# Performance work log

Hardware: AMD Instinct MI355X
Metric: run time of the kernel (lower is better)

Reference implementation:

```python
import jax, jax.numpy as jnp
import numpy as np

N = 50000
E = 1600000
R = 4
D_IN = 128
D_OUT = 128


def setup_inputs() -> dict:
    key = jax.random.key(0)
    ks = jax.random.split(key, 7)
    x = jax.random.normal(ks[0], (N, D_IN), dtype=jnp.float32)
    vals = jax.random.normal(ks[1], (R, E), dtype=jnp.float32) * (1.0 / 32.0)
    weight = jax.random.normal(ks[2], (D_IN, D_OUT), dtype=jnp.float32) * (1.0 / np.sqrt(D_IN))
    filt = jax.random.uniform(ks[3], (R * N, 1), dtype=jnp.float32, minval=0.9, maxval=1.1)
    bias = jnp.zeros((D_OUT,), dtype=jnp.float32)
    rows = jax.random.randint(ks[4], (R, E), 0, N, dtype=jnp.int32)
    cols = jax.random.randint(ks[5], (R, E), 0, N, dtype=jnp.int32)
    return {"x": x, "vals": vals, "weight": weight, "filt": filt,
            "bias": bias, "rows": rows, "cols": cols}


def _spmm(rows, cols, vals, h, n):
    # sparse [n,n] @ dense [n,d] via gather + segment_sum
    return jax.ops.segment_sum(vals[:, None] * h[cols], rows, num_segments=n)


def reference(x, vals, weight, filt, bias, rows, cols):
    n = x.shape[0]
    h = x @ weight                                    # [N, out]
    # cat(d_list, dim=0) @ h  ->  stack of D_i @ h, i.e. [R, N, out]
    y = jax.vmap(lambda r, c, v: _spmm(r, c, v, h, n))(rows, cols, vals)
    y = filt.reshape(rows.shape[0], n, 1) * y         # elementwise wavelet filter
    # cat(d_list, dim=1) @ y  ->  sum_i D_i @ y_i
    out = jax.vmap(lambda r, c, v, yy: _spmm(r, c, v, yy, n))(rows, cols, vals, y).sum(axis=0)
    return out + bias
```

## Files before the change

kernel.cpp:

```cpp
#include <hip/hip_runtime.h>

#define N_NODES 50000
#define N_EDGES 1600000
#define R_WAV 4
#define D 128
#define NB 391
#define CHUNK 4096
#define NPBLK ((N_EDGES + CHUNK - 1) / CHUNK)
#define MAXB 4800

typedef unsigned int u32;
typedef unsigned short u16;

static __device__ inline u16 f2bf(float f) {
    u32 u = __float_as_uint(f);
    u = (u + 0x7FFFu + ((u >> 16) & 1u)) >> 16;
    return (u16)u;
}
static __device__ inline float bf_lo(u32 u) { return __uint_as_float(u << 16); }
static __device__ inline float bf_hi(u32 u) { return __uint_as_float(u & 0xFFFF0000u); }

__global__ __launch_bounds__(128) void gemm_xw(const float* __restrict__ x,
                                               const float* __restrict__ W,
                                               u16* __restrict__ h) {
    __shared__ float xs[4 * 128];
    const int j = threadIdx.x;
    const int row0 = blockIdx.x * 4;
    for (int t = j; t < 512; t += 128) xs[t] = x[(size_t)row0 * D + t];
    __syncthreads();
    float a0 = 0.f, a1 = 0.f, a2 = 0.f, a3 = 0.f;
#pragma unroll 8
    for (int k = 0; k < 128; ++k) {
        const float w = W[k * D + j];
        a0 += xs[k] * w;
        a1 += xs[128 + k] * w;
        a2 += xs[256 + k] * w;
        a3 += xs[384 + k] * w;
    }
    h[(size_t)(row0 + 0) * D + j] = f2bf(a0);
    h[(size_t)(row0 + 1) * D + j] = f2bf(a1);
    h[(size_t)(row0 + 2) * D + j] = f2bf(a2);
    h[(size_t)(row0 + 3) * D + j] = f2bf(a3);
}

__global__ __launch_bounds__(256) void bucket_hist_all(const int* __restrict__ rows_all,
                                                       int* __restrict__ cnt4) {
    __shared__ int lh[NB];
    const int r = blockIdx.y;
    const int* rows = rows_all + (size_t)r * N_EDGES;
    int* cnt = cnt4 + r * NB;
    const int tid = threadIdx.x;
    for (int i = tid; i < NB; i += 256) lh[i] = 0;
    __syncthreads();
    const int e0 = blockIdx.x * CHUNK;
    const int e1 = min(e0 + CHUNK, N_EDGES);
    for (int i = e0 + tid; i < e1; i += 256) atomicAdd(&lh[rows[i] >> 7], 1);
    __syncthreads();
    for (int i = tid; i < NB; i += 256) {
        const int c = lh[i];
        if (c) atomicAdd(&cnt[i], c);
    }
}

__global__ __launch_bounds__(512) void scan_buckets_all(const int* __restrict__ cnt4,
                                                        int* __restrict__ bptr4,
                                                        int* __restrict__ bcur4) {
    __shared__ int sa[512], sb[512];
    const int r = blockIdx.x;
    const int* cnt = cnt4 + r * NB;
    int* bptr = bptr4 + r * (NB + 1);
    int* bcur = bcur4 + r * NB;
    const int tid = threadIdx.x;
    const int v = (tid < NB) ? cnt[tid] : 0;
    sa[tid] = v;
    int* cur = sa;
    int* nxt = sb;
    for (int d = 1; d < 512; d <<= 1) {
        __syncthreads();
        int t = cur[tid];
        if (tid >= d) t += cur[tid - d];
        nxt[tid] = t;
        int* tmp = cur; cur = nxt; nxt = tmp;
    }
    __syncthreads();
    const int excl = cur[tid] - v;
    if (tid <= NB) bptr[tid] = excl;
    if (tid < NB) bcur[tid] = excl;
}

__global__ __launch_bounds__(256) void partition_kernel(const int* __restrict__ rows,
                                                        const int* __restrict__ cols,
                                                        const float* __restrict__ vals,
                                                        int* __restrict__ bcur,
                                                        int2* __restrict__ cv) {
    __shared__ int lh[NB], lptr[NB], lcur[NB], lbase[NB];
    __shared__ int sa[256], sb[256];
    __shared__ int2 st[CHUNK];
    const int tid = threadIdx.x;
    for (int i = tid; i < NB; i += 256) lh[i] = 0;
    __syncthreads();
    const int e0 = blockIdx.x * CHUNK;
    const int e1 = min(e0 + CHUNK, N_EDGES);
    const int cnt = e1 - e0;
    for (int i = e0 + tid; i < e1; i += 256) atomicAdd(&lh[rows[i] >> 7], 1);
    __syncthreads();
    const int p0 = (2 * tid < NB) ? lh[2 * tid] : 0;
    const int p1 = (2 * tid + 1 < NB) ? lh[2 * tid + 1] : 0;
    sa[tid] = p0 + p1;
    int* cur = sa;
    int* nxt = sb;
    for (int d = 1; d < 256; d <<= 1) {
        __syncthreads();
        int t = cur[tid];
        if (tid >= d) t += cur[tid - d];
        nxt[tid] = t;
        int* tmp = cur; cur = nxt; nxt = tmp;
    }
    __syncthreads();
    const int pe = cur[tid] - (p0 + p1);
    if (2 * tid < NB)     { lptr[2 * tid] = pe;           lcur[2 * tid] = pe; }
    if (2 * tid + 1 < NB) { lptr[2 * tid + 1] = pe + p0;  lcur[2 * tid + 1] = pe + p0; }
    __syncthreads();
    for (int i = e0 + tid; i < e1; i += 256) {
        const int row = rows[i];
        const int b = row >> 7;
        const int pos = atomicAdd(&lcur[b], 1);
        st[pos] = make_int2((int)(((u32)row << 16) | (u32)cols[i]), __float_as_int(vals[i]));
    }
    __syncthreads();
    for (int b = tid; b < NB; b += 256) {
        const int c = lh[b];
        int gb = 0;
        if (c) gb = atomicAdd(&bcur[b], c);
        lbase[b] = gb - lptr[b];
    }
    __syncthreads();
    for (int i = tid; i < cnt; i += 256) {
        const int2 e = st[i];
        const int b = (int)((u32)e.x >> 23);
        cv[lbase[b] + i] = e;
    }
}

__global__ __launch_bounds__(256) void bucket_csr(const int* __restrict__ bptr,
                                                  const int2* __restrict__ cv,
                                                  u32* __restrict__ cv4,
                                                  int* __restrict__ row_ptr) {
    __shared__ int lh[128], lexcl[128], lcur[128];
    __shared__ u32 st[MAXB];
    const int b = blockIdx.x;
    const int s = bptr[b], e1 = bptr[b + 1];
    const int cnt = e1 - s;
    const int tid = threadIdx.x;
    if (tid < 128) lh[tid] = 0;
    __syncthreads();
    for (int i = s + tid; i < e1; i += 256)
        atomicAdd(&lh[((u32)cv[i].x >> 16) & 127u], 1);
    __syncthreads();
    if (tid < 64) {
        const int p0 = lh[2 * tid], p1 = lh[2 * tid + 1];
        int ssum = p0 + p1;
#pragma unroll
        for (int d = 1; d < 64; d <<= 1) {
            const int t = __shfl_up(ssum, d, 64);
            if (tid >= d) ssum += t;
        }
        const int pe = ssum - (p0 + p1);
        lexcl[2 * tid] = pe;          lcur[2 * tid] = pe;
        lexcl[2 * tid + 1] = pe + p0; lcur[2 * tid + 1] = pe + p0;
    }
    __syncthreads();
    for (int i = s + tid; i < e1; i += 256) {
        const int2 E = cv[i];
        const int lr = (int)(((u32)E.x >> 16) & 127u);
        const int pos = atomicAdd(&lcur[lr], 1);
        if (pos < MAXB)
            st[pos] = ((u32)f2bf(__int_as_float(E.y)) << 16) | ((u32)E.x & 0xFFFFu);
    }
    __syncthreads();
    const int wb = (cnt < MAXB) ? cnt : MAXB;
    for (int i = tid; i < wb; i += 256) cv4[s + i] = st[i];
    if (tid < 128) {
        const int row = (b << 7) + tid;
        if (row < N_NODES) row_ptr[row] = s + lexcl[tid];
    }
    if (b == 0 && tid == 0) row_ptr[N_NODES] = N_EDGES;
}

__global__ __launch_bounds__(256) void spmm1(const int* __restrict__ row_ptr,
                                             const u32* __restrict__ cvp,
                                             const u32* __restrict__ h2,
                                             const float* __restrict__ filt_r,
                                             u32* __restrict__ y2) {
    const int row = __builtin_amdgcn_readfirstlane(blockIdx.x * 4 + (threadIdx.x >> 6));
    const int lane = threadIdx.x & 63;
    const int half = lane >> 5;
    const int l = lane & 31;
    int e = row_ptr[row];
    const int end = row_ptr[row + 1];
    float a0 = 0.f, a1 = 0.f, a2 = 0.f, a3 = 0.f;
    float b0 = 0.f, b1 = 0.f, b2 = 0.f, b3 = 0.f;
    for (; e + 8 <= end; e += 8) {
        const u32 c0 = cvp[e], c1 = cvp[e + 1], c2 = cvp[e + 2], c3 = cvp[e + 3];
        const u32 c4 = cvp[e + 4], c5 = cvp[e + 5], c6 = cvp[e + 6], c7 = cvp[e + 7];
        const u32 uA = half ? c1 : c0;
        const u32 uB = half ? c3 : c2;
        const u32 uC = half ? c5 : c4;
        const u32 uD = half ? c7 : c6;
        const uint2 gA = *(const uint2*)(h2 + (uA & 0xFFFFu) * 64 + 2 * l);
        const uint2 gB = *(const uint2*)(h2 + (uB & 0xFFFFu) * 64 + 2 * l);
        const uint2 gC = *(const uint2*)(h2 + (uC & 0xFFFFu) * 64 + 2 * l);
        const uint2 gD = *(const uint2*)(h2 + (uD & 0xFFFFu) * 64 + 2 * l);
        const float vA = __uint_as_float(uA & 0xFFFF0000u);
        const float vB = __uint_as_float(uB & 0xFFFF0000u);
        const float vC = __uint_as_float(uC & 0xFFFF0000u);
        const float vD = __uint_as_float(uD & 0xFFFF0000u);
        a0 += vA * bf_lo(gA.x); a1 += vA * bf_hi(gA.x);
        a2 += vA * bf_lo(gA.y); a3 += vA * bf_hi(gA.y);
        b0 += vB * bf_lo(gB.x); b1 += vB * bf_hi(gB.x);
        b2 += vB * bf_lo(gB.y); b3 += vB * bf_hi(gB.y);
        a0 += vC * bf_lo(gC.x); a1 += vC * bf_hi(gC.x);
        a2 += vC * bf_lo(gC.y); a3 += vC * bf_hi(gC.y);
        b0 += vD * bf_lo(gD.x); b1 += vD * bf_hi(gD.x);
        b2 += vD * bf_lo(gD.y); b3 += vD * bf_hi(gD.y);
    }
    for (; e < end; e += 2) {
        const u32 c0 = cvp[e];
        const u32 c1 = (e + 1 < end) ? cvp[e + 1] : 0u;
        const u32 uA = half ? c1 : c0;
        const uint2 gA = *(const uint2*)(h2 + (uA & 0xFFFFu) * 64 + 2 * l);
        const float vA = __uint_as_float(uA & 0xFFFF0000u);
        a0 += vA * bf_lo(gA.x); a1 += vA * bf_hi(gA.x);
        a2 += vA * bf_lo(gA.y); a3 += vA * bf_hi(gA.y);
    }
    a0 += b0; a1 += b1; a2 += b2; a3 += b3;
    a0 += __shfl_xor(a0, 32, 64);
    a1 += __shfl_xor(a1, 32, 64);
    a2 += __shfl_xor(a2, 32, 64);
    a3 += __shfl_xor(a3, 32, 64);
    const float f = filt_r[row];
    if (half == 0) {
        uint2 o;
        o.x = (u32)f2bf(f * a0) | ((u32)f2bf(f * a1) << 16);
        o.y = (u32)f2bf(f * a2) | ((u32)f2bf(f * a3) << 16);
        *(uint2*)(y2 + (size_t)row * 64 + 2 * l) = o;
    }
}

template <bool FIRST>
__global__ __launch_bounds__(256) void spmm2(const int* __restrict__ row_ptr,
                                             const u32* __restrict__ cvp,
                                             const u32* __restrict__ y2,
                                             const float* __restrict__ bias,
                                             float* __restrict__ out) {
    const int row = __builtin_amdgcn_readfirstlane(blockIdx.x * 4 + (threadIdx.x >> 6));
    const int lane = threadIdx.x & 63;
    const int half = lane >> 5;
    const int l = lane & 31;
    int e = row_ptr[row];
    const int end = row_ptr[row + 1];
    float a0 = 0.f, a1 = 0.f, a2 = 0.f, a3 = 0.f;
    float b0 = 0.f, b1 = 0.f, b2 = 0.f, b3 = 0.f;
    for (; e + 8 <= end; e += 8) {
        const u32 c0 = cvp[e], c1 = cvp[e + 1], c2 = cvp[e + 2], c3 = cvp[e + 3];
        const u32 c4 = cvp[e + 4], c5 = cvp[e + 5], c6 = cvp[e + 6], c7 = cvp[e + 7];
        const u32 uA = half ? c1 : c0;
        const u32 uB = half ? c3 : c2;
        const u32 uC = half ? c5 : c4;
        const u32 uD = half ? c7 : c6;
        const uint2 gA = *(const uint2*)(y2 + (uA & 0xFFFFu) * 64 + 2 * l);
        const uint2 gB = *(const uint2*)(y2 + (uB & 0xFFFFu) * 64 + 2 * l);
        const uint2 gC = *(const uint2*)(y2 + (uC & 0xFFFFu) * 64 + 2 * l);
        const uint2 gD = *(const uint2*)(y2 + (uD & 0xFFFFu) * 64 + 2 * l);
        const float vA = __uint_as_float(uA & 0xFFFF0000u);
        const float vB = __uint_as_float(uB & 0xFFFF0000u);
        const float vC = __uint_as_float(uC & 0xFFFF0000u);
        const float vD = __uint_as_float(uD & 0xFFFF0000u);
        a0 += vA * bf_lo(gA.x); a1 += vA * bf_hi(gA.x);
        a2 += vA * bf_lo(gA.y); a3 += vA * bf_hi(gA.y);
        b0 += vB * bf_lo(gB.x); b1 += vB * bf_hi(gB.x);
        b2 += vB * bf_lo(gB.y); b3 += vB * bf_hi(gB.y);
        a0 += vC * bf_lo(gC.x); a1 += vC * bf_hi(gC.x);
        a2 += vC * bf_lo(gC.y); a3 += vC * bf_hi(gC.y);
        b0 += vD * bf_lo(gD.x); b1 += vD * bf_hi(gD.x);
        b2 += vD * bf_lo(gD.y); b3 += vD * bf_hi(gD.y);
    }
    for (; e < end; e += 2) {
        const u32 c0 = cvp[e];
        const u32 c1 = (e + 1 < end) ? cvp[e + 1] : 0u;
        const u32 uA = half ? c1 : c0;
        const uint2 gA = *(const uint2*)(y2 + (uA & 0xFFFFu) * 64 + 2 * l);
        const float vA = __uint_as_float(uA & 0xFFFF0000u);
        a0 += vA * bf_lo(gA.x); a1 += vA * bf_hi(gA.x);
        a2 += vA * bf_lo(gA.y); a3 += vA * bf_hi(gA.y);
    }
    a0 += b0; a1 += b1; a2 += b2; a3 += b3;
    a0 += __shfl_xor(a0, 32, 64);
    a1 += __shfl_xor(a1, 32, 64);
    a2 += __shfl_xor(a2, 32, 64);
    a3 += __shfl_xor(a3, 32, 64);
    if (half == 0) {
        float* op = out + (size_t)row * D + 4 * l;
        if (FIRST) {
            const float4 bb = *(const float4*)(bias + 4 * l);
            *(float4*)op = make_float4(a0 + bb.x, a1 + bb.y, a2 + bb.z, a3 + bb.w);
        } else {
            const float4 cc = *(const float4*)op;
            *(float4*)op = make_float4(cc.x + a0, cc.y + a1, cc.z + a2, cc.w + a3);
        }
    }
}

extern "C" void kernel_launch(void* const* d_in, const int* in_sizes, int n_in,
                              void* d_out, int out_size, void* d_ws, size_t ws_size,
                              hipStream_t stream) {
    const float* x    = (const float*)d_in[0];
    const float* vals = (const float*)d_in[1];
    const float* W    = (const float*)d_in[2];
    const float* filt = (const float*)d_in[3];
    const float* bias = (const float*)d_in[4];
    const int*   rows = (const int*)d_in[5];
    const int*   cols = (const int*)d_in[6];
    float* out = (float*)d_out;

    char* ws = (char*)d_ws;
    u16*  h       = (u16*)(ws);
    u32*  y2      = (u32*)(ws + 12800000);
    int2* cv8     = (int2*)(ws + 25600000);
    u32*  cv4     = (u32*)(ws + 38400000);
    int*  row_ptr = (int*)(ws + 44800512);
    int*  cnt4    = (int*)(ws + 45000576);
    int*  bptr4   = (int*)(ws + 45006976);
    int*  bcur4   = (int*)(ws + 45013376);

    gemm_xw<<<N_NODES / 4, 128, 0, stream>>>(x, W, h);

    hipMemsetAsync(cnt4, 0, 4 * NB * sizeof(int), stream);
    bucket_hist_all<<<dim3(NPBLK, R_WAV), 256, 0, stream>>>(rows, cnt4);
    scan_buckets_all<<<R_WAV, 512, 0, stream>>>(cnt4, bptr4, bcur4);

    for (int r = 0; r < R_WAV; ++r) {
        const int*   rows_r = rows + (size_t)r * N_EDGES;
        const int*   cols_r = cols + (size_t)r * N_EDGES;
        const float* vals_r = vals + (size_t)r * N_EDGES;
        const float* filt_r = filt + (size_t)r * N_NODES;

        partition_kernel<<<NPBLK, 256, 0, stream>>>(rows_r, cols_r, vals_r,
                                                    bcur4 + r * NB, cv8);
        bucket_csr<<<NB, 256, 0, stream>>>(bptr4 + r * (NB + 1), cv8, cv4, row_ptr);
        spmm1<<<N_NODES / 4, 256, 0, stream>>>(row_ptr, cv4, (const u32*)h, filt_r, y2);
        if (r == 0)
            spmm2<true><<<N_NODES / 4, 256, 0, stream>>>(row_ptr, cv4, y2, bias, out);
        else
            spmm2<false><<<N_NODES / 4, 256, 0, stream>>>(row_ptr, cv4, y2, bias, out);
    }
}
```

Baseline: 734.2 us.

## Batch all wavelets per launch and fuse second SpMM across wavelets

When the workspace is large enough, partition, CSR build and the first SpMM run for all four wavelets in single launches via blockIdx.y, with per-wavelet buffers. The second SpMM is fused into one kernel that loops over the four wavelets per row, accumulates in registers and writes the output once, instead of four read-modify-write passes over the output. The GEMM is also changed to compute 16 rows per block reading x directly rather than 4 rows via shared memory. The cost is a much larger workspace, and a fallback keeps the old per-wavelet path when it is too small.

```diff
diff --git a/kernel.cpp b/kernel.cpp
--- a/kernel.cpp
+++ b/kernel.cpp
@@ -8,6 +8,7 @@
 #define CHUNK 4096
 #define NPBLK ((N_EDGES + CHUNK - 1) / CHUNK)
 #define MAXB 4800
+#define RP_STRIDE 50016
 
 typedef unsigned int u32;
 typedef unsigned short u16;
@@ -23,24 +24,20 @@
 __global__ __launch_bounds__(128) void gemm_xw(const float* __restrict__ x,
                                                const float* __restrict__ W,
                                                u16* __restrict__ h) {
-    __shared__ float xs[4 * 128];
     const int j = threadIdx.x;
-    const int row0 = blockIdx.x * 4;
-    for (int t = j; t < 512; t += 128) xs[t] = x[(size_t)row0 * D + t];
-    __syncthreads();
-    float a0 = 0.f, a1 = 0.f, a2 = 0.f, a3 = 0.f;
-#pragma unroll 8
+    const int row0 = blockIdx.x * 16;
+    const float* xr = x + (size_t)row0 * D;
+    float acc[16];
+#pragma unroll
+    for (int r = 0; r < 16; ++r) acc[r] = 0.f;
+#pragma unroll 4
     for (int k = 0; k < 128; ++k) {
         const float w = W[k * D + j];
-        a0 += xs[k] * w;
-        a1 += xs[128 + k] * w;
-        a2 += xs[256 + k] * w;
-        a3 += xs[384 + k] * w;
-    }
-    h[(size_t)(row0 + 0) * D + j] = f2bf(a0);
-    h[(size_t)(row0 + 1) * D + j] = f2bf(a1);
-    h[(size_t)(row0 + 2) * D + j] = f2bf(a2);
-    h[(size_t)(row0 + 3) * D + j] = f2bf(a3);
+#pragma unroll
+        for (int r = 0; r < 16; ++r) acc[r] += xr[r * D + k] * w;
+    }
+#pragma unroll
+    for (int r = 0; r < 16; ++r) h[(size_t)(row0 + r) * D + j] = f2bf(acc[r]);
 }
 
 __global__ __launch_bounds__(256) void bucket_hist_all(const int* __restrict__ rows_all,
@@ -93,6 +90,12 @@
                                                         const float* __restrict__ vals,
                                                         int* __restrict__ bcur,
                                                         int2* __restrict__ cv) {
+    const int r = blockIdx.y;
+    rows += (size_t)r * N_EDGES;
+    cols += (size_t)r * N_EDGES;
+    vals += (size_t)r * N_EDGES;
+    bcur += r * NB;
+    cv   += (size_t)r * N_EDGES;
     __shared__ int lh[NB], lptr[NB], lcur[NB], lbase[NB];
     __shared__ int sa[256], sb[256];
     __shared__ int2 st[CHUNK];
@@ -146,6 +149,11 @@
                                                   const int2* __restrict__ cv,
                                                   u32* __restrict__ cv4,
                                                   int* __restrict__ row_ptr) {
+    const int r = blockIdx.y;
+    bptr    += r * (NB + 1);
+    cv      += (size_t)r * N_EDGES;
+    cv4     += (size_t)r * N_EDGES;
+    row_ptr += r * RP_STRIDE;
     __shared__ int lh[128], lexcl[128], lcur[128];
     __shared__ u32 st[MAXB];
     const int b = blockIdx.x;
@@ -184,14 +192,19 @@
         const int row = (b << 7) + tid;
         if (row < N_NODES) row_ptr[row] = s + lexcl[tid];
     }
-    if (b == 0 && tid == 0) row_ptr[N_NODES] = N_EDGES;
+    if (blockIdx.x == 0 && tid == 0) row_ptr[N_NODES] = N_EDGES;
 }
 
 __global__ __launch_bounds__(256) void spmm1(const int* __restrict__ row_ptr,
                                              const u32* __restrict__ cvp,
                                              const u32* __restrict__ h2,
-                                             const float* __restrict__ filt_r,
+                                             const float* __restrict__ filt,
                                              u32* __restrict__ y2) {
+    const int r = blockIdx.y;
+    row_ptr += r * RP_STRIDE;
+    cvp     += (size_t)r * N_EDGES;
+    filt    += (size_t)r * N_NODES;
+    y2      += (size_t)r * (N_NODES * 64);
     const int row = __builtin_amdgcn_readfirstlane(blockIdx.x * 4 + (threadIdx.x >> 6));
     const int lane = threadIdx.x & 63;
     const int half = lane >> 5;
@@ -238,12 +251,75 @@
     a1 += __shfl_xor(a1, 32, 64);
     a2 += __shfl_xor(a2, 32, 64);
     a3 += __shfl_xor(a3, 32, 64);
-    const float f = filt_r[row];
+    const float f = filt[row];
     if (half == 0) {
         uint2 o;
         o.x = (u32)f2bf(f * a0) | ((u32)f2bf(f * a1) << 16);
         o.y = (u32)f2bf(f * a2) | ((u32)f2bf(f * a3) << 16);
         *(uint2*)(y2 + (size_t)row * 64 + 2 * l) = o;
+    }
+}
+
+__global__ __launch_bounds__(256) void spmm2_fused(const int* __restrict__ rp_all,
+                                                   const u32* __restrict__ cv4_all,
+                                                   const u32* __restrict__ y2_all,
+                                                   const float* __restrict__ bias,
+                                                   float* __restrict__ out) {
+    const int row = __builtin_amdgcn_readfirstlane(blockIdx.x * 4 + (threadIdx.x >> 6));
+    const int lane = threadIdx.x & 63;
+    const int half = lane >> 5;
+    const int l = lane & 31;
+    float a0 = 0.f, a1 = 0.f, a2 = 0.f, a3 = 0.f;
+    float b0 = 0.f, b1 = 0.f, b2 = 0.f, b3 = 0.f;
+    for (int r = 0; r < R_WAV; ++r) {
+        const int* rp = rp_all + r * RP_STRIDE;
+        const u32* cvp = cv4_all + (size_t)r * N_EDGES;
+        const u32* y2 = y2_all + (size_t)r * (N_NODES * 64);
+        int e = rp[row];
+        const int end = rp[row + 1];
+        for (; e + 8 <= end; e += 8) {
+            const u32 c0 = cvp[e], c1 = cvp[e + 1], c2 = cvp[e + 2], c3 = cvp[e + 3];
+            const u32 c4 = cvp[e + 4], c5 = cvp[e + 5], c6 = cvp[e + 6], c7 = cvp[e + 7];
+            const u32 uA = half ? c1 : c0;
+            const u32 uB = half ? c3 : c2;
+            const u32 uC = half ? c5 : c4;
+            const u32 uD = half ? c7 : c6;
+            const uint2 gA = *(const uint2*)(y2 + (uA & 0xFFFFu) * 64 + 2 * l);
+            const uint2 gB = *(const uint2*)(y2 + (uB & 0xFFFFu) * 64 + 2 * l);
+            const uint2 gC = *(const uint2*)(y2 + (uC & 0xFFFFu) * 64 + 2 * l);
+            const uint2 gD = *(const uint2*)(y2 + (uD & 0xFFFFu) * 64 + 2 * l);
+            const float vA = __uint_as_float(uA & 0xFFFF0000u);
+            const float vB = __uint_as_float(uB & 0xFFFF0000u);
+            const float vC = __uint_as_float(uC & 0xFFFF0000u);
+            const float vD = __uint_as_float(uD & 0xFFFF0000u);
+            a0 += vA * bf_lo(gA.x); a1 += vA * bf_hi(gA.x);
+            a2 += vA * bf_lo(gA.y); a3 += vA * bf_hi(gA.y);
+            b0 += vB * bf_lo(gB.x); b1 += vB * bf_hi(gB.x);
+            b2 += vB * bf_lo(gB.y); b3 += vB * bf_hi(gB.y);
+            a0 += vC * bf_lo(gC.x); a1 += vC * bf_hi(gC.x);
+            a2 += vC * bf_lo(gC.y); a3 += vC * bf_hi(gC.y);
+            b0 += vD * bf_lo(gD.x); b1 += vD * bf_hi(gD.x);
+            b2 += vD * bf_lo(gD.y); b3 += vD * bf_hi(gD.y);
+        }
+        for (; e < end; e += 2) {
+            const u32 c0 = cvp[e];
+            const u32 c1 = (e + 1 < end) ? cvp[e + 1] : 0u;
+            const u32 uA = half ? c1 : c0;
+            const uint2 gA = *(const uint2*)(y2 + (uA & 0xFFFFu) * 64 + 2 * l);
+            const float vA = __uint_as_float(uA & 0xFFFF0000u);
+            a0 += vA * bf_lo(gA.x); a1 += vA * bf_hi(gA.x);
+            a2 += vA * bf_lo(gA.y); a3 += vA * bf_hi(gA.y);
+        }
+    }
+    a0 += b0; a1 += b1; a2 += b2; a3 += b3;
+    a0 += __shfl_xor(a0, 32, 64);
+    a1 += __shfl_xor(a1, 32, 64);
+    a2 += __shfl_xor(a2, 32, 64);
+    a3 += __shfl_xor(a3, 32, 64);
+    if (half == 0) {
+        const float4 bb = *(const float4*)(bias + 4 * l);
+        *(float4*)(out + (size_t)row * D + 4 * l) =
+            make_float4(a0 + bb.x, a1 + bb.y, a2 + bb.z, a3 + bb.w);
     }
 }
 
@@ -324,34 +400,63 @@
     float* out = (float*)d_out;
 
     char* ws = (char*)d_ws;
-    u16*  h       = (u16*)(ws);
-    u32*  y2      = (u32*)(ws + 12800000);
-    int2* cv8     = (int2*)(ws + 25600000);
-    u32*  cv4     = (u32*)(ws + 38400000);
-    int*  row_ptr = (int*)(ws + 44800512);
-    int*  cnt4    = (int*)(ws + 45000576);
-    int*  bptr4   = (int*)(ws + 45006976);
-    int*  bcur4   = (int*)(ws + 45013376);
-
-    gemm_xw<<<N_NODES / 4, 128, 0, stream>>>(x, W, h);
-
-    hipMemsetAsync(cnt4, 0, 4 * NB * sizeof(int), stream);
-    bucket_hist_all<<<dim3(NPBLK, R_WAV), 256, 0, stream>>>(rows, cnt4);
-    scan_buckets_all<<<R_WAV, 512, 0, stream>>>(cnt4, bptr4, bcur4);
-
-    for (int r = 0; r < R_WAV; ++r) {
-        const int*   rows_r = rows + (size_t)r * N_EDGES;
-        const int*   cols_r = cols + (size_t)r * N_EDGES;
-        const float* vals_r = vals + (size_t)r * N_EDGES;
-        const float* filt_r = filt + (size_t)r * N_NODES;
-
-        partition_kernel<<<NPBLK, 256, 0, stream>>>(rows_r, cols_r, vals_r,
-                                                    bcur4 + r * NB, cv8);
-        bucket_csr<<<NB, 256, 0, stream>>>(bptr4 + r * (NB + 1), cv8, cv4, row_ptr);
-        spmm1<<<N_NODES / 4, 256, 0, stream>>>(row_ptr, cv4, (const u32*)h, filt_r, y2);
-        if (r == 0)
-            spmm2<true><<<N_NODES / 4, 256, 0, stream>>>(row_ptr, cv4, y2, bias, out);
-        else
-            spmm2<false><<<N_NODES / 4, 256, 0, stream>>>(row_ptr, cv4, y2, bias, out);
-    }
-}
+    const size_t NEED_BATCHED = 90419968;
+
+    if (ws_size >= NEED_BATCHED) {
+        u16*  h   = (u16*)(ws);
+        u32*  sh  = (u32*)(ws + 12800000);
+        int2* cv8 = (int2*)sh;
+        u32*  y2  = sh;
+        u32*  cv4 = (u32*)(ws + 64000000);
+        int*  rp  = (int*)(ws + 89600000);
+        int*  cnt4  = (int*)(ws + 90400512);
+        int*  bptr4 = (int*)(ws + 90406912);
+        int*  bcur4 = (int*)(ws + 90413312);
+
+        gemm_xw<<<N_NODES / 16, 128, 0, stream>>>(x, W, h);
+
+        hipMemsetAsync(cnt4, 0, 4 * NB * sizeof(int), stream);
+        bucket_hist_all<<<dim3(NPBLK, R_WAV), 256, 0, stream>>>(rows, cnt4);
+        scan_buckets_all<<<R_WAV, 512, 0, stream>>>(cnt4, bptr4, bcur4);
+
+        partition_kernel<<<dim3(NPBLK, R_WAV), 256, 0, stream>>>(rows, cols, vals,
+                                                                 bcur4, cv8);
+        bucket_csr<<<dim3(NB, R_WAV), 256, 0, stream>>>(bptr4, cv8, cv4, rp);
+        spmm1<<<dim3(N_NODES / 4, R_WAV), 256, 0, stream>>>(rp, cv4, (const u32*)h,
+                                                            filt, y2);
+        spmm2_fused<<<N_NODES / 4, 256, 0, stream>>>(rp, cv4, y2, bias, out);
+    } else {
+        u16*  h       = (u16*)(ws);
+        u32*  y2      = (u32*)(ws + 12800000);
+        int2* cv8     = (int2*)(ws + 25600000);
+        u32*  cv4     = (u32*)(ws + 38400000);
+        int*  row_ptr = (int*)(ws + 44800512);
+        int*  cnt4    = (int*)(ws + 45000576);
+        int*  bptr4   = (int*)(ws + 45006976);
+        int*  bcur4   = (int*)(ws + 45013376);
+
+        gemm_xw<<<N_NODES / 16, 128, 0, stream>>>(x, W, h);
+
+        hipMemsetAsync(cnt4, 0, 4 * NB * sizeof(int), stream);
+        bucket_hist_all<<<dim3(NPBLK, R_WAV), 256, 0, stream>>>(rows, cnt4);
+        scan_buckets_all<<<R_WAV, 512, 0, stream>>>(cnt4, bptr4, bcur4);
+
+        for (int r = 0; r < R_WAV; ++r) {
+            const int*   rows_r = rows + (size_t)r * N_EDGES;
+            const int*   cols_r = cols + (size_t)r * N_EDGES;
+            const float* vals_r = vals + (size_t)r * N_EDGES;
+            const float* filt_r = filt + (size_t)r * N_NODES;
+
+            partition_kernel<<<dim3(NPBLK, 1), 256, 0, stream>>>(rows_r, cols_r, vals_r,
+                                                                 bcur4 + r * NB, cv8);
+            bucket_csr<<<dim3(NB, 1), 256, 0, stream>>>(bptr4 + r * (NB + 1), cv8,
+                                                        cv4, row_ptr);
+            spmm1<<<dim3(N_NODES / 4, 1), 256, 0, stream>>>(row_ptr, cv4, (const u32*)h,
+                                                            filt_r, y2);
+            if (r == 0)
+                spmm2<true><<<N_NODES / 4, 256, 0, stream>>>(row_ptr, cv4, y2, bias, out);
+            else
+                spmm2<false><<<N_NODES / 4, 256, 0, stream>>>(row_ptr, cv4, y2, bias, out);
+        }
+    }
+}
```

After: 719.7 us. -2.0%, faster.
